# Performance work log

Measured on AMD Instinct MI355X. Metric: run time of the kernel, lower is better.

Reference implementation:

```python
import jax, jax.numpy as jnp
import numpy as np

DIM = 512
N_HEADS = 8
D_HEAD = 64            # NOTE: module splits heads by d_head (64 heads of dim 8) - faithful to source
ENC_DIM = 768
GN_GROUPS = 32
EPS = 1e-5


def setup_inputs() -> dict:
    key = jax.random.key(0)
    ks = jax.random.split(key, 12)
    B, H, W = 2, 32, 32
    w = lambda k, s: jax.random.normal(k, s, dtype=jnp.float32) * 0.02
    return {
        "hidden_states": jax.random.normal(ks[0], (B, H, W, DIM), dtype=jnp.float32),
        "encoder_hidden_states": jax.random.normal(ks[1], (B, 77, ENC_DIM), dtype=jnp.float32),
        "gn_scale": jnp.ones((DIM,), jnp.float32),
        "gn_bias": jnp.zeros((DIM,), jnp.float32),
        "ln_scale": jnp.ones((ENC_DIM,), jnp.float32),
        "ln_bias": jnp.zeros((ENC_DIM,), jnp.float32),
        "Wq": w(ks[2], (DIM, DIM)), "bq": jnp.zeros((DIM,), jnp.float32),
        "Wk": w(ks[3], (DIM, DIM)), "bk": jnp.zeros((DIM,), jnp.float32),
        "Wv": w(ks[4], (DIM, DIM)), "bv": jnp.zeros((DIM,), jnp.float32),
        "Wak": w(ks[5], (ENC_DIM, DIM)), "bak": jnp.zeros((DIM,), jnp.float32),
        "Wav": w(ks[6], (ENC_DIM, DIM)), "bav": jnp.zeros((DIM,), jnp.float32),
        "Wo": w(ks[7], (DIM, DIM)), "bo": jnp.zeros((DIM,), jnp.float32),
    }


def _group_norm(x, scale, bias):
    # x: [B, N, C]; flax GroupNorm: stats over (N, C/group) per group
    B, N, C = x.shape
    g = x.reshape(B, N, GN_GROUPS, C // GN_GROUPS)
    mu = g.mean(axis=(1, 3), keepdims=True)
    var = g.var(axis=(1, 3), keepdims=True)
    g = (g - mu) * jax.lax.rsqrt(var + EPS)
    return g.reshape(B, N, C) * scale + bias


def _layer_norm(x, scale, bias):
    mu = x.mean(-1, keepdims=True)
    var = x.var(-1, keepdims=True)
    return (x - mu) * jax.lax.rsqrt(var + EPS) * scale + bias


def _split_heads(t):
    # head_to_batch_dim(out_dim=4) with head_size = D_HEAD (faithful to source)
    B, S, D = t.shape
    return t.reshape(B, S, D_HEAD, D // D_HEAD).transpose(0, 2, 1, 3)  # [B, 64, S, 8]


def reference(hidden_states, encoder_hidden_states, gn_scale, gn_bias, ln_scale, ln_bias,
              Wq, bq, Wk, bk, Wv, bv, Wak, bak, Wav, bav, Wo, bo):
    B, H, W, C = hidden_states.shape
    residual = jnp.transpose(hidden_states, (0, 3, 1, 2))            # [B, C, H, W]
    hs = jnp.transpose(residual.reshape(B, C, H * W), (0, 2, 1))     # [B, N, C]

    enc = _layer_norm(encoder_hidden_states, ln_scale, ln_bias)      # norm_cross
    hs = _group_norm(hs, gn_scale, gn_bias)

    q = _split_heads(hs @ Wq + bq)                                   # [B, 64, N, 8]
    k_self = _split_heads(hs @ Wk + bk)
    v_self = _split_heads(hs @ Wv + bv)
    k_enc = _split_heads(enc @ Wak + bak)                            # [B, 64, 77, 8]
    v_enc = _split_heads(enc @ Wav + bav)

    k = jnp.concatenate([k_enc, k_self], axis=2)                     # [B, 64, 77+N, 8]
    v = jnp.concatenate([v_enc, v_self], axis=2)

    scale = 1.0 / jnp.sqrt(jnp.float32(q.shape[-1]))
    scores = jnp.einsum('bhid,bhjd->bhij', q, k) * scale             # [B, 64, N, 77+N]
    probs = jax.nn.softmax(scores, axis=-1)
    out = jnp.einsum('bhij,bhjd->bhid', probs, v)                    # [B, 64, N, 8]

    out = jnp.transpose(out, (0, 2, 1, 3)).reshape(B, H * W, C)
    out = out @ Wo + bo                                              # to_out[0]
    out = jnp.transpose(out, (0, 2, 1)).reshape(residual.shape)      # [B, C, H, W]
    out = out + residual
    # source does a raw reshape (not transpose) back to NHWC shape - keep faithful
    return out.reshape(hidden_states.shape)
```

## Files before the change

### kernel.cpp

```cpp
#include <hip/hip_runtime.h>
#include <math.h>

#define BSZ   2
#define NTOK  1024
#define CDIM  512
#define SENC  77
#define SKV   1101
#define KROWS 1120
#define ENCD  768
#define NHEAD 64
#define DHEAD 8

typedef short short8 __attribute__((ext_vector_type(8)));
typedef float floatx4 __attribute__((ext_vector_type(4)));
typedef unsigned short ushortx4 __attribute__((ext_vector_type(4)));

__device__ __forceinline__ unsigned short f2bf(float f) {
    union { float f; unsigned int u; } v; v.f = f;
    unsigned int r = v.u + 0x7FFF + ((v.u >> 16) & 1);
    return (unsigned short)(r >> 16);
}
__device__ __forceinline__ unsigned short rtzbf(float f) {
    return (unsigned short)(__float_as_uint(f) >> 16);
}

__device__ __forceinline__ void gld16(const void* g, void* l) {
    __builtin_amdgcn_global_load_lds(
        (const __attribute__((address_space(1))) unsigned int*)g,
        (__attribute__((address_space(3))) unsigned int*)l,
        16, 0, 0);
}

__device__ __forceinline__ float block_reduce_sum(float v) {
    #pragma unroll
    for (int off = 32; off > 0; off >>= 1) v += __shfl_down(v, off, 64);
    __shared__ float tmp[4];
    int lane = threadIdx.x & 63, wid = threadIdx.x >> 6;
    if (lane == 0) tmp[wid] = v;
    __syncthreads();
    if (wid == 0) {
        float r = (lane < 4) ? tmp[lane] : 0.f;
        r += __shfl_down(r, 2, 64);
        r += __shfl_down(r, 1, 64);
        if (lane == 0) tmp[0] = r;
    }
    __syncthreads();
    float out = tmp[0];
    __syncthreads();
    return out;
}

__device__ void layernorm_dev(int row, const float* __restrict__ x,
                              const float* __restrict__ sc, const float* __restrict__ bi,
                              unsigned short* __restrict__ out) {
    const float* xp = x + (size_t)row * ENCD;
    unsigned short* op = out + (size_t)row * ENCD;
    int t = threadIdx.x;
    float v0 = xp[t], v1 = xp[t + 256], v2 = xp[t + 512];
    float mu = block_reduce_sum(v0 + v1 + v2) * (1.f / ENCD);
    float d0 = v0 - mu, d1 = v1 - mu, d2 = v2 - mu;
    float var = block_reduce_sum(d0 * d0 + d1 * d1 + d2 * d2) * (1.f / ENCD);
    float rstd = rsqrtf(var + 1e-5f);
    op[t]       = f2bf(d0 * rstd * sc[t]       + bi[t]);
    op[t + 256] = f2bf(d1 * rstd * sc[t + 256] + bi[t + 256]);
    op[t + 512] = f2bf(d2 * rstd * sc[t + 512] + bi[t + 512]);
}

__device__ void groupnorm_dev(int bg, const float* __restrict__ x,
                              const float* __restrict__ sc, const float* __restrict__ bi,
                              unsigned short* __restrict__ out) {
    int b = bg >> 5, g = bg & 31;
    const float* xp = x + (size_t)b * NTOK * CDIM + g * 16;
    unsigned short* op = out + (size_t)b * NTOK * CDIM + g * 16;
    int t = threadIdx.x;
    int q = t & 3;

    float4 v[16];
    #pragma unroll
    for (int it = 0; it < 16; ++it) {
        int idx = t + it * 256;
        int n = idx >> 2;
        v[it] = *(const float4*)(xp + n * CDIM + q * 4);
    }
    float s = 0.f, ss = 0.f;
    #pragma unroll
    for (int it = 0; it < 16; ++it) {
        s  += (v[it].x + v[it].y) + (v[it].z + v[it].w);
        ss += (v[it].x * v[it].x + v[it].y * v[it].y)
            + (v[it].z * v[it].z + v[it].w * v[it].w);
    }
    float mu  = block_reduce_sum(s)  * (1.f / 16384.f);
    float msq = block_reduce_sum(ss) * (1.f / 16384.f);
    float rstd = rsqrtf(msq - mu * mu + 1e-5f);

    float4 s4 = *(const float4*)(sc + g * 16 + q * 4);
    float4 b4 = *(const float4*)(bi + g * 16 + q * 4);
    #pragma unroll
    for (int it = 0; it < 16; ++it) {
        int idx = t + it * 256;
        int n = idx >> 2;
        ushortx4 o;
        o[0] = f2bf((v[it].x - mu) * rstd * s4.x + b4.x);
        o[1] = f2bf((v[it].y - mu) * rstd * s4.y + b4.y);
        o[2] = f2bf((v[it].z - mu) * rstd * s4.z + b4.z);
        o[3] = f2bf((v[it].w - mu) * rstd * s4.w + b4.w);
        *(ushortx4*)(op + n * CDIM + q * 4) = o;
    }
}

__device__ void tcast_dev(const float* __restrict__ W, unsigned short* __restrict__ Wt,
                          int K, int N, int roff, int local) {
    __shared__ float t[32][33];
    int bn = (local & 15) * 32, bk = (local >> 4) * 32;
    int lx = threadIdx.x & 31, ly = threadIdx.x >> 5;
    #pragma unroll
    for (int r = 0; r < 4; ++r)
        t[ly + 8 * r][lx] = W[(size_t)(bk + ly + 8 * r) * N + bn + lx];
    __syncthreads();
    #pragma unroll
    for (int r = 0; r < 4; ++r)
        Wt[(size_t)(roff + bn + ly + 8 * r) * K + bk + lx] = f2bf(t[lx][ly + 8 * r]);
}

__global__ __launch_bounds__(256) void prep_all(
        const float* __restrict__ Wq, const float* __restrict__ Wk, const float* __restrict__ Wv,
        const float* __restrict__ Wak, const float* __restrict__ Wav, const float* __restrict__ Wo,
        const float* __restrict__ bq, const float* __restrict__ bk, const float* __restrict__ bv,
        const float* __restrict__ bak, const float* __restrict__ bav,
        const float* __restrict__ enc, const float* __restrict__ ln_s, const float* __restrict__ ln_b,
        const float* __restrict__ x, const float* __restrict__ gn_s, const float* __restrict__ gn_b,
        unsigned short* __restrict__ Wqkv_t, unsigned short* __restrict__ Wakv_t,
        unsigned short* __restrict__ Wo_t,
        float* __restrict__ bqkv, float* __restrict__ bakv,
        unsigned short* __restrict__ enc_bf, unsigned short* __restrict__ hs_bf,
        unsigned short* __restrict__ Vh) {
    int bid = blockIdx.x;
    if (bid < 256)        tcast_dev(Wq,  Wqkv_t, 512, 512, 0,    bid);
    else if (bid < 512)   tcast_dev(Wk,  Wqkv_t, 512, 512, 512,  bid - 256);
    else if (bid < 768)   tcast_dev(Wv,  Wqkv_t, 512, 512, 1024, bid - 512);
    else if (bid < 1152)  tcast_dev(Wak, Wakv_t, 768, 512, 0,    bid - 768);
    else if (bid < 1536)  tcast_dev(Wav, Wakv_t, 768, 512, 512,  bid - 1152);
    else if (bid < 1792)  tcast_dev(Wo,  Wo_t,   512, 512, 0,    bid - 1536);
    else if (bid < 1802) {
        int i = (bid - 1792) * 256 + threadIdx.x;
        if (i < 512)        bqkv[i] = bq[i];
        else if (i < 1024)  bqkv[i] = bk[i - 512];
        else if (i < 1536)  bqkv[i] = bv[i - 1024];
        else if (i < 2048)  bakv[i - 1536] = bak[i - 1536];
        else if (i < 2560)  bakv[i - 1536] = bav[i - 2048];
    }
    else if (bid < 1956)  layernorm_dev(bid - 1802, enc, ln_s, ln_b, enc_bf);
    else if (bid < 2020)  groupnorm_dev(bid - 1956, x, gn_s, gn_b, hs_bf);
    else {
        int i = (bid - 2020) * 256 + threadIdx.x;
        int g = i / KROWS, kv = i - g * KROWS;
        Vh[((size_t)g * 16 + 8) * KROWS + kv] = 0x3F80;
    }
}

template <bool SWAP>
__device__ __forceinline__ void gemm_core(
        const unsigned short* __restrict__ A, int Mv,
        const unsigned short* __restrict__ Bt, int K,
        int m0, int n0, unsigned short* AsS, unsigned short* BsS,
        floatx4 (&acc)[4][4]) {
    int tid = threadIdx.x;
    int wv = tid >> 6, ln = tid & 63;
    int quad = ln >> 4, l16 = ln & 15;
    int wr = wv >> 1, wc = wv & 1;

    for (int k0 = 0; k0 < K; k0 += 32) {
        #pragma unroll
        for (int it = 0; it < 2; ++it) {
            int cb = it * 256 + wv * 64;
            int c = cb + ln;
            int r = c >> 2, sg = c & 3;
            int row = m0 + r; if (row > Mv - 1) row = Mv - 1;
            gld16((const void*)(A + (size_t)row * K + k0 + sg * 8),
                  (void*)((char*)AsS + cb * 16));
            gld16((const void*)(Bt + (size_t)(n0 + r) * K + k0 + sg * 8),
                  (void*)((char*)BsS + cb * 16));
        }
        __syncthreads();
        short8 af[4], bf[4];
        #pragma unroll
        for (int i = 0; i < 4; ++i)
            af[i] = *(const short8*)(AsS + (wr * 64 + i * 16 + l16) * 32 + quad * 8);
        #pragma unroll
        for (int j = 0; j < 4; ++j)
            bf[j] = *(const short8*)(BsS + (wc * 64 + j * 16 + l16) * 32 + quad * 8);
        #pragma unroll
        for (int i = 0; i < 4; ++i)
            #pragma unroll
            for (int j = 0; j < 4; ++j)
                acc[i][j] = SWAP
                    ? __builtin_amdgcn_mfma_f32_16x16x32_bf16(bf[j], af[i], acc[i][j], 0, 0, 0)
                    : __builtin_amdgcn_mfma_f32_16x16x32_bf16(af[i], bf[j], acc[i][j], 0, 0, 0);
        __syncthreads();
    }
}

__global__ __launch_bounds__(256) void proj_gemm(
        const unsigned short* __restrict__ hs_bf, const unsigned short* __restrict__ enc_bf,
        const unsigned short* __restrict__ Wqkv_t, const unsigned short* __restrict__ Wakv_t,
        const float* __restrict__ bqkv, const float* __restrict__ bakv,
        unsigned short* __restrict__ Qh, unsigned short* __restrict__ Kh,
        unsigned short* __restrict__ Vh) {
    __shared__ alignas(16) unsigned short AsS[128 * 32];
    __shared__ alignas(16) unsigned short BsS[128 * 32];
    floatx4 acc[4][4] = {};
    int bid = blockIdx.x;
    int tid = threadIdx.x;
    int wv = tid >> 6, ln = tid & 63;
    int quad = ln >> 4, l16 = ln & 15;
    int wr = wv >> 1, wc = wv & 1;
    const float ASCALE = 0.3535533905932738f * 1.4426950408889634f;

    if (bid < 192) {
        int n0 = (bid % 12) * 128, m0 = (bid / 12) * 128;
        gemm_core<true>(hs_bf, 2048, Wqkv_t, 512, m0, n0, AsS, BsS, acc);
        #pragma unroll
        for (int i = 0; i < 4; ++i) {
            int tok = m0 + wr * 64 + i * 16 + l16;
            int b_ = tok >> 10, nn = tok & 1023;
            #pragma unroll
            for (int j = 0; j < 4; ++j) {
                int colb = n0 + wc * 64 + j * 16 + quad * 4;
                float vv[4];
                #pragma unroll
                for (int r = 0; r < 4; ++r) vv[r] = acc[i][j][r] + bqkv[colb + r];
                if (colb < 512) {
                    int h = colb >> 3, c = colb & 7;
                    ushortx4 w = { f2bf(vv[0] * ASCALE), f2bf(vv[1] * ASCALE),
                                   f2bf(vv[2] * ASCALE), f2bf(vv[3] * ASCALE) };
                    *(ushortx4*)(Qh + ((size_t)(b_ * 64 + h) * 1024 + nn) * 8 + c) = w;
                } else if (colb < 1024) {
                    int cc = colb - 512, h = cc >> 3, c = cc & 7;
                    ushortx4 w = { f2bf(vv[0]), f2bf(vv[1]), f2bf(vv[2]), f2bf(vv[3]) };
                    *(ushortx4*)(Kh + ((size_t)(b_ * 64 + h) * KROWS + nn) * 8 + c) = w;
                } else {
                    int cc = colb - 1024, h = cc >> 3, c = cc & 7;
                    #pragma unroll
                    for (int r = 0; r < 4; ++r)
                        Vh[((size_t)(b_ * 64 + h) * 16 + c + r) * KROWS + nn] = f2bf(vv[r]);
                }
            }
        }
    } else {
        int idx = bid - 192;
        int n0 = (idx % 8) * 128, m0 = (idx / 8) * 128;
        gemm_core<true>(enc_bf, 154, Wakv_t, 768, m0, n0, AsS, BsS, acc);
        #pragma unroll
        for (int i = 0; i < 4; ++i) {
            int rg = m0 + wr * 64 + i * 16 + l16;
            bool ok = rg < 154;
            int b_ = rg >= 77;
            int jj = rg - 77 * b_;
            #pragma unroll
            for (int j = 0; j < 4; ++j) {
                int colb = n0 + wc * 64 + j * 16 + quad * 4;
                float vv[4];
                #pragma unroll
                for (int r = 0; r < 4; ++r) vv[r] = acc[i][j][r] + bakv[colb + r];
                if (colb < 512) {
                    int h = colb >> 3, c = colb & 7;
                    if (ok) {
                        ushortx4 w = { f2bf(vv[0]), f2bf(vv[1]), f2bf(vv[2]), f2bf(vv[3]) };
                        *(ushortx4*)(Kh + ((size_t)(b_ * 64 + h) * KROWS + 1024 + jj) * 8 + c) = w;
                    }
                } else {
                    int cc = colb - 512, h = cc >> 3, c = cc & 7;
                    if (ok) {
                        #pragma unroll
                        for (int r = 0; r < 4; ++r)
                            Vh[((size_t)(b_ * 64 + h) * 16 + c + r) * KROWS + 1024 + jj] = f2bf(vv[r]);
                    }
                }
            }
        }
    }
}

__global__ __launch_bounds__(256) void gemm_out(
        const unsigned short* __restrict__ Wo_t, const unsigned short* __restrict__ AO,
        const float* __restrict__ bias, const float* __restrict__ resid,
        float* __restrict__ out) {
    __shared__ alignas(16) unsigned short AsS[128 * 32];
    __shared__ alignas(16) unsigned short BsS[128 * 32];
    floatx4 acc[4][4] = {};
    int tid = threadIdx.x;
    int wv = tid >> 6, ln = tid & 63;
    int quad = ln >> 4, l16 = ln & 15;
    int wr = wv >> 1, wc = wv & 1;
    int n0 = blockIdx.x * 128, m0 = blockIdx.y * 128;
    gemm_core<false>(Wo_t, 512, AO, 512, m0, n0, AsS, BsS, acc);
    #pragma unroll
    for (int i = 0; i < 4; ++i) {
        int cbase = m0 + wr * 64 + i * 16 + quad * 4;
        #pragma unroll
        for (int j = 0; j < 4; ++j) {
            int ng = n0 + wc * 64 + j * 16 + l16;
            int b = ng >> 10, n = ng & 1023;
            float4 res = *(const float4*)(resid + ((size_t)(b * 1024 + n)) * 512 + cbase);
            float rr[4] = {res.x, res.y, res.z, res.w};
            #pragma unroll
            for (int r = 0; r < 4; ++r) {
                int c = cbase + r;
                out[((size_t)(b * 512 + c)) * 1024 + n] = acc[i][j][r] + bias[c] + rr[r];
            }
        }
    }
}

__global__ __launch_bounds__(256) void attn_mfma(
        const unsigned short* __restrict__ Qh,
        const unsigned short* __restrict__ Kh,
        const unsigned short* __restrict__ Vh,
        unsigned short* __restrict__ AO) {
    __shared__ alignas(16) unsigned short P_lds[4][2][16][40];
    int x = blockIdx.x;
    int h = x & 63, qt = (x >> 6) & 7, b = x >> 9;
    int tid = threadIdx.x, wv = tid >> 6, ln = tid & 63;
    int quad = ln >> 4, l16 = ln & 15;
    int q0r = qt * 128 + wv * 32;
    int bh = b * 64 + h;

    short8 qa = {}, qb = {};
    if (quad == 0) {
        qa = *(const short8*)(Qh + ((size_t)bh * 1024 + q0r + l16) * 8);
        qb = *(const short8*)(Qh + ((size_t)bh * 1024 + q0r + 16 + l16) * 8);
    }
    const unsigned short* Kb = Kh + (size_t)bh * KROWS * 8;
    const unsigned short* Vb = Vh + ((size_t)bh * 16 + l16) * KROWS;

    floatx4 acca = {}, accb = {};
    unsigned short* Pa = &P_lds[wv][0][0][0];
    unsigned short* Pb = &P_lds[wv][1][0][0];

    for (int base = 0; base < 1088; base += 32) {
        short8 k0 = *(const short8*)(Kb + (size_t)(base + l16) * 8);
        short8 k1 = *(const short8*)(Kb + (size_t)(base + 16 + l16) * 8);
        short8 vf = *(const short8*)(Vb + base + quad * 8);
        floatx4 z = {};
        floatx4 s0a = __builtin_amdgcn_mfma_f32_16x16x32_bf16(k0, qa, z, 0, 0, 0);
        floatx4 s1a = __builtin_amdgcn_mfma_f32_16x16x32_bf16(k1, qa, z, 0, 0, 0);
        floatx4 s0b = __builtin_amdgcn_mfma_f32_16x16x32_bf16(k0, qb, z, 0, 0, 0);
        floatx4 s1b = __builtin_amdgcn_mfma_f32_16x16x32_bf16(k1, qb, z, 0, 0, 0);
        ushortx4 w0a, w1a, w0b, w1b;
        #pragma unroll
        for (int r = 0; r < 4; ++r) {
            w0a[r] = rtzbf(__builtin_amdgcn_exp2f(s0a[r]));
            w1a[r] = rtzbf(__builtin_amdgcn_exp2f(s1a[r]));
            w0b[r] = rtzbf(__builtin_amdgcn_exp2f(s0b[r]));
            w1b[r] = rtzbf(__builtin_amdgcn_exp2f(s1b[r]));
        }
        *(ushortx4*)(Pa + l16 * 40 + quad * 4)      = w0a;
        *(ushortx4*)(Pa + l16 * 40 + 16 + quad * 4) = w1a;
        *(ushortx4*)(Pb + l16 * 40 + quad * 4)      = w0b;
        *(ushortx4*)(Pb + l16 * 40 + 16 + quad * 4) = w1b;
        short8 pfa = *(const short8*)(Pa + l16 * 40 + quad * 8);
        short8 pfb = *(const short8*)(Pb + l16 * 40 + quad * 8);
        acca = __builtin_amdgcn_mfma_f32_16x16x32_bf16(pfa, vf, acca, 0, 0, 0);
        accb = __builtin_amdgcn_mfma_f32_16x16x32_bf16(pfb, vf, accb, 0, 0, 0);
    }
    {
        short8 k0 = *(const short8*)(Kb + (size_t)(1088 + l16) * 8);
        short8 vf = *(const short8*)(Vb + 1088 + quad * 8);
        floatx4 z = {};
        floatx4 s0a = __builtin_amdgcn_mfma_f32_16x16x32_bf16(k0, qa, z, 0, 0, 0);
        floatx4 s0b = __builtin_amdgcn_mfma_f32_16x16x32_bf16(k0, qb, z, 0, 0, 0);
        ushortx4 w0a, w0b, wz;
        #pragma unroll
        for (int r = 0; r < 4; ++r) {
            bool valid = (quad * 4 + r) < 13;
            w0a[r] = valid ? rtzbf(__builtin_amdgcn_exp2f(s0a[r])) : (unsigned short)0;
            w0b[r] = valid ? rtzbf(__builtin_amdgcn_exp2f(s0b[r])) : (unsigned short)0;
            wz[r] = 0;
        }
        *(ushortx4*)(Pa + l16 * 40 + quad * 4)      = w0a;
        *(ushortx4*)(Pa + l16 * 40 + 16 + quad * 4) = wz;
        *(ushortx4*)(Pb + l16 * 40 + quad * 4)      = w0b;
        *(ushortx4*)(Pb + l16 * 40 + 16 + quad * 4) = wz;
        short8 pfa = *(const short8*)(Pa + l16 * 40 + quad * 8);
        short8 pfb = *(const short8*)(Pb + l16 * 40 + quad * 8);
        acca = __builtin_amdgcn_mfma_f32_16x16x32_bf16(pfa, vf, acca, 0, 0, 0);
        accb = __builtin_amdgcn_mfma_f32_16x16x32_bf16(pfb, vf, accb, 0, 0, 0);
    }

    #pragma unroll
    for (int r = 0; r < 4; ++r) {
        float la = __shfl(acca[r], (ln & 48) + 8, 64);
        float lb = __shfl(accb[r], (ln & 48) + 8, 64);
        if (l16 < 8) {
            AO[((size_t)(b * 1024 + q0r + quad * 4 + r)) * 512 + h * 8 + l16] =
                f2bf(acca[r] / la);
            AO[((size_t)(b * 1024 + q0r + 16 + quad * 4 + r)) * 512 + h * 8 + l16] =
                f2bf(accb[r] / lb);
        }
    }
}

extern "C" void kernel_launch(void* const* d_in, const int* in_sizes, int n_in,
                              void* d_out, int out_size, void* d_ws, size_t ws_size,
                              hipStream_t stream) {
    const float* x    = (const float*)d_in[0];
    const float* enc  = (const float*)d_in[1];
    const float* gn_s = (const float*)d_in[2];
    const float* gn_b = (const float*)d_in[3];
    const float* ln_s = (const float*)d_in[4];
    const float* ln_b = (const float*)d_in[5];
    const float* Wq  = (const float*)d_in[6];   const float* bq  = (const float*)d_in[7];
    const float* Wk  = (const float*)d_in[8];   const float* bk  = (const float*)d_in[9];
    const float* Wv  = (const float*)d_in[10];  const float* bv  = (const float*)d_in[11];
    const float* Wak = (const float*)d_in[12];  const float* bak = (const float*)d_in[13];
    const float* Wav = (const float*)d_in[14];  const float* bav = (const float*)d_in[15];
    const float* Wo  = (const float*)d_in[16];  const float* bo  = (const float*)d_in[17];
    float* out = (float*)d_out;

    char* p = (char*)d_ws;
    auto alloc = [&](size_t bytes) { char* r = p; p += (bytes + 255) & ~255ULL; return r; };
    unsigned short* hs_bf  = (unsigned short*)alloc((size_t)2048 * 512 * 2);
    unsigned short* enc_bf = (unsigned short*)alloc((size_t)154 * 768 * 2);
    unsigned short* Wqkv_t = (unsigned short*)alloc((size_t)1536 * 512 * 2);
    unsigned short* Wakv_t = (unsigned short*)alloc((size_t)1024 * 768 * 2);
    unsigned short* Wo_t   = (unsigned short*)alloc((size_t)512 * 512 * 2);
    float* bqkv = (float*)alloc(1536 * 4);
    float* bakv = (float*)alloc(1024 * 4);
    unsigned short* Qh = (unsigned short*)alloc((size_t)2 * 64 * 1024 * 8 * 2);
    unsigned short* Kh = (unsigned short*)alloc((size_t)2 * 64 * KROWS * 8 * 2);
    unsigned short* Vh = (unsigned short*)alloc((size_t)2 * 64 * 16 * KROWS * 2);
    unsigned short* AO = (unsigned short*)alloc((size_t)2048 * 512 * 2);

    prep_all<<<2580, 256, 0, stream>>>(
        Wq, Wk, Wv, Wak, Wav, Wo, bq, bk, bv, bak, bav,
        enc, ln_s, ln_b, x, gn_s, gn_b,
        Wqkv_t, Wakv_t, Wo_t, bqkv, bakv, enc_bf, hs_bf, Vh);

    proj_gemm<<<208, 256, 0, stream>>>(
        hs_bf, enc_bf, Wqkv_t, Wakv_t, bqkv, bakv, Qh, Kh, Vh);

    attn_mfma<<<BSZ * NHEAD * 8, 256, 0, stream>>>(Qh, Kh, Vh, AO);

    gemm_out<<<dim3(16, 4), 256, 0, stream>>>(Wo_t, AO, bo, x, out);

    (void)in_sizes; (void)n_in; (void)out_size; (void)ws_size;
}
```

Measured before the change: 156.2 us.

## Permute V key order so P stays in registers, removing LDS round-trip

The QKV projection epilogue now writes V columns in a permuted key order within each 32-key block, matching the register layout of the exp'd score MFMA output. The attention kernel then packs the probabilities directly into the MFMA A operand instead of writing them to shared memory and reading them back. This removes per-iteration LDS stores and loads and the shared P buffer. It relies on the permutation exactly matching the MFMA fragment layout, including for the padded tail block.

Measured after the change: 154.2 us. Within noise of the previous version (-1.2%).

```diff
diff --git a/kernel.cpp b/kernel.cpp
--- a/kernel.cpp
+++ b/kernel.cpp
@@ -22,6 +22,9 @@
 }
 __device__ __forceinline__ unsigned short rtzbf(float f) {
     return (unsigned short)(__float_as_uint(f) >> 16);
+}
+__device__ __forceinline__ int vslot(int kr) {
+    return ((kr & 12) << 1) | ((kr & 16) >> 2) | (kr & 3);
 }
 
 __device__ __forceinline__ void gld16(const void* g, void* l) {
@@ -223,6 +226,7 @@
         for (int i = 0; i < 4; ++i) {
             int tok = m0 + wr * 64 + i * 16 + l16;
             int b_ = tok >> 10, nn = tok & 1023;
+            int vcol = (nn & ~31) | vslot(nn & 31);
             #pragma unroll
             for (int j = 0; j < 4; ++j) {
                 int colb = n0 + wc * 64 + j * 16 + quad * 4;
@@ -242,7 +246,7 @@
                     int cc = colb - 1024, h = cc >> 3, c = cc & 7;
                     #pragma unroll
                     for (int r = 0; r < 4; ++r)
-                        Vh[((size_t)(b_ * 64 + h) * 16 + c + r) * KROWS + nn] = f2bf(vv[r]);
+                        Vh[((size_t)(b_ * 64 + h) * 16 + c + r) * KROWS + vcol] = f2bf(vv[r]);
                 }
             }
         }
@@ -256,6 +260,8 @@
             bool ok = rg < 154;
             int b_ = rg >= 77;
             int jj = rg - 77 * b_;
+            int e = 1024 + jj;
+            int vcol = (e & ~31) | vslot(e & 31);
             #pragma unroll
             for (int j = 0; j < 4; ++j) {
                 int colb = n0 + wc * 64 + j * 16 + quad * 4;
@@ -273,7 +279,7 @@
                     if (ok) {
                         #pragma unroll
                         for (int r = 0; r < 4; ++r)
-                            Vh[((size_t)(b_ * 64 + h) * 16 + c + r) * KROWS + 1024 + jj] = f2bf(vv[r]);
+                            Vh[((size_t)(b_ * 64 + h) * 16 + c + r) * KROWS + vcol] = f2bf(vv[r]);
                     }
                 }
             }
@@ -317,7 +323,6 @@
         const unsigned short* __restrict__ Kh,
         const unsigned short* __restrict__ Vh,
         unsigned short* __restrict__ AO) {
-    __shared__ alignas(16) unsigned short P_lds[4][2][16][40];
     int x = blockIdx.x;
     int h = x & 63, qt = (x >> 6) & 7, b = x >> 9;
     int tid = threadIdx.x, wv = tid >> 6, ln = tid & 63;
@@ -334,8 +339,6 @@
     const unsigned short* Vb = Vh + ((size_t)bh * 16 + l16) * KROWS;
 
     floatx4 acca = {}, accb = {};
-    unsigned short* Pa = &P_lds[wv][0][0][0];
-    unsigned short* Pb = &P_lds[wv][1][0][0];
 
     for (int base = 0; base < 1088; base += 32) {
         short8 k0 = *(const short8*)(Kb + (size_t)(base + l16) * 8);
@@ -346,22 +349,16 @@
         floatx4 s1a = __builtin_amdgcn_mfma_f32_16x16x32_bf16(k1, qa, z, 0, 0, 0);
         floatx4 s0b = __builtin_amdgcn_mfma_f32_16x16x32_bf16(k0, qb, z, 0, 0, 0);
         floatx4 s1b = __builtin_amdgcn_mfma_f32_16x16x32_bf16(k1, qb, z, 0, 0, 0);
-        ushortx4 w0a, w1a, w0b, w1b;
+        union { ushortx4 hlf[2]; short8 s; } ua, ub;
         #pragma unroll
         for (int r = 0; r < 4; ++r) {
-            w0a[r] = rtzbf(__builtin_amdgcn_exp2f(s0a[r]));
-            w1a[r] = rtzbf(__builtin_amdgcn_exp2f(s1a[r]));
-            w0b[r] = rtzbf(__builtin_amdgcn_exp2f(s0b[r]));
-            w1b[r] = rtzbf(__builtin_amdgcn_exp2f(s1b[r]));
-        }
-        *(ushortx4*)(Pa + l16 * 40 + quad * 4)      = w0a;
-        *(ushortx4*)(Pa + l16 * 40 + 16 + quad * 4) = w1a;
-        *(ushortx4*)(Pb + l16 * 40 + quad * 4)      = w0b;
-        *(ushortx4*)(Pb + l16 * 40 + 16 + quad * 4) = w1b;
-        short8 pfa = *(const short8*)(Pa + l16 * 40 + quad * 8);
-        short8 pfb = *(const short8*)(Pb + l16 * 40 + quad * 8);
-        acca = __builtin_amdgcn_mfma_f32_16x16x32_bf16(pfa, vf, acca, 0, 0, 0);
-        accb = __builtin_amdgcn_mfma_f32_16x16x32_bf16(pfb, vf, accb, 0, 0, 0);
+            ua.hlf[0][r] = rtzbf(__builtin_amdgcn_exp2f(s0a[r]));
+            ua.hlf[1][r] = rtzbf(__builtin_amdgcn_exp2f(s1a[r]));
+            ub.hlf[0][r] = rtzbf(__builtin_amdgcn_exp2f(s0b[r]));
+            ub.hlf[1][r] = rtzbf(__builtin_amdgcn_exp2f(s1b[r]));
+        }
+        acca = __builtin_amdgcn_mfma_f32_16x16x32_bf16(ua.s, vf, acca, 0, 0, 0);
+        accb = __builtin_amdgcn_mfma_f32_16x16x32_bf16(ub.s, vf, accb, 0, 0, 0);
     }
     {
         short8 k0 = *(const short8*)(Kb + (size_t)(1088 + l16) * 8);
@@ -369,22 +366,17 @@
         floatx4 z = {};
         floatx4 s0a = __builtin_amdgcn_mfma_f32_16x16x32_bf16(k0, qa, z, 0, 0, 0);
         floatx4 s0b = __builtin_amdgcn_mfma_f32_16x16x32_bf16(k0, qb, z, 0, 0, 0);
-        ushortx4 w0a, w0b, wz;
+        union { ushortx4 hlf[2]; short8 s; } ua, ub;
         #pragma unroll
         for (int r = 0; r < 4; ++r) {
             bool valid = (quad * 4 + r) < 13;
-            w0a[r] = valid ? rtzbf(__builtin_amdgcn_exp2f(s0a[r])) : (unsigned short)0;
-            w0b[r] = valid ? rtzbf(__builtin_amdgcn_exp2f(s0b[r])) : (unsigned short)0;
-            wz[r] = 0;
-        }
-        *(ushortx4*)(Pa + l16 * 40 + quad * 4)      = w0a;
-        *(ushortx4*)(Pa + l16 * 40 + 16 + quad * 4) = wz;
-        *(ushortx4*)(Pb + l16 * 40 + quad * 4)      = w0b;
-        *(ushortx4*)(Pb + l16 * 40 + 16 + quad * 4) = wz;
-        short8 pfa = *(const short8*)(Pa + l16 * 40 + quad * 8);
-        short8 pfb = *(const short8*)(Pb + l16 * 40 + quad * 8);
-        acca = __builtin_amdgcn_mfma_f32_16x16x32_bf16(pfa, vf, acca, 0, 0, 0);
-        accb = __builtin_amdgcn_mfma_f32_16x16x32_bf16(pfb, vf, accb, 0, 0, 0);
+            ua.hlf[0][r] = valid ? rtzbf(__builtin_amdgcn_exp2f(s0a[r])) : (unsigned short)0;
+            ua.hlf[1][r] = 0;
+            ub.hlf[0][r] = valid ? rtzbf(__builtin_amdgcn_exp2f(s0b[r])) : (unsigned short)0;
+            ub.hlf[1][r] = 0;
+        }
+        acca = __builtin_amdgcn_mfma_f32_16x16x32_bf16(ua.s, vf, acca, 0, 0, 0);
+        accb = __builtin_amdgcn_mfma_f32_16x16x32_bf16(ub.s, vf, accb, 0, 0, 0);
     }
 
     #pragma unroll
```
